# Kernel optimization log

Hardware: AMD Instinct MI355X
Metric: run time of the kernel (lower is better)

The kernel has to match this reference:

```python
import jax, jax.numpy as jnp
import numpy as np

N_NODES = 50000
N_EDGES = 800000
N_FEAT = 128
HIDDEN = 64


def gcn_conv(x, W, b, src, dst, n_nodes):
    """PyG GCNConv: h = D^{-1/2}(A+I)D^{-1/2} (x @ W) + b, with self-loops."""
    h = x @ W  # [N, H] -- linear first, then aggregate (as PyG does)
    # degree including self-loop: deg[i] = 1 + in-degree(i)
    deg = jnp.ones((n_nodes,), dtype=h.dtype).at[dst].add(1.0)
    dinv = jax.lax.rsqrt(deg)  # deg >= 1 so safe
    # edge messages with symmetric normalization
    coef = dinv[src] * dinv[dst]  # [E]
    msg = h[src] * coef[:, None]  # [E, H]  (dominant memory traffic)
    agg = jnp.zeros_like(h).at[dst].add(msg)
    # self-loop contribution: dinv[i]^2 * h[i]
    out = agg + h * (dinv * dinv)[:, None]
    return out + b


def setup_inputs() -> dict:
    key = jax.random.key(0)
    k1, k2, k3, k4 = jax.random.split(key, 4)
    x = jax.random.normal(k1, (N_NODES, N_FEAT), dtype=jnp.float32)
    edge_index = jax.random.randint(k2, (2, N_EDGES), 0, N_NODES, dtype=jnp.int64)
    W1 = jax.random.normal(k3, (N_FEAT, HIDDEN), dtype=jnp.float32) / np.sqrt(N_FEAT)
    b1 = jnp.zeros((HIDDEN,), dtype=jnp.float32)
    W2 = jax.random.normal(k4, (HIDDEN, HIDDEN), dtype=jnp.float32) / np.sqrt(HIDDEN)
    b2 = jnp.zeros((HIDDEN,), dtype=jnp.float32)
    return {"x": x, "edge_index": edge_index, "W1": W1, "b1": b1, "W2": W2, "b2": b2}


def reference(x, edge_index, W1, b1, W2, b2):
    # eval mode: F.dropout(p=0.5, training=False) is identity
    src, dst = edge_index[0], edge_index[1]
    h = gcn_conv(x, W1, b1, src, dst, N_NODES)
    h = jax.nn.relu(h)
    h = gcn_conv(h, W2, b2, src, dst, N_NODES)
    h = jax.nn.relu(h)
    return h
```

## Files before the change

kernel.cpp:

```cpp
#include <hip/hip_runtime.h>
#include <hip/hip_bf16.h>
#include <hip/hip_fp16.h>


#define THREADS 256

__device__ inline int wave_incl_scan(int v, int lane) {
#pragma unroll
    for (int ofs = 1; ofs < 64; ofs <<= 1) {
        int t = __shfl_up(v, ofs, 64);
        if (lane >= ofs) v += t;
    }
    return v;
}

__global__ void k_zero(int4* __restrict__ p, int n4) {
    int i = blockIdx.x * blockDim.x + threadIdx.x;
    if (i < n4) p[i] = make_int4(0, 0, 0, 0);
}

__global__ __launch_bounds__(256)
void k_bin_count(const int* __restrict__ dst, int* __restrict__ bincnt,
                 int n_edges) {
    __shared__ int hist[1024];
    const int tid = threadIdx.x;
    for (int i = tid; i < 1024; i += 256) hist[i] = 0;
    __syncthreads();
    const int base = blockIdx.x * 4096 + tid * 16;
#pragma unroll
    for (int j = 0; j < 4; ++j) {
        int o = base + j * 4;
        if (o + 4 <= n_edges) {
            int4 d = *(const int4*)&dst[o];
            atomicAdd(&hist[d.x >> 6], 1);
            atomicAdd(&hist[d.y >> 6], 1);
            atomicAdd(&hist[d.z >> 6], 1);
            atomicAdd(&hist[d.w >> 6], 1);
        } else {
            for (int t = o; t < n_edges; ++t) atomicAdd(&hist[dst[t] >> 6], 1);
        }
    }
    __syncthreads();
    for (int i = tid; i < 1024; i += 256)
        if (hist[i]) atomicAdd(&bincnt[i], hist[i]);
}

__global__ __launch_bounds__(1024)
void k_bin_scan(const int* __restrict__ bincnt, int* __restrict__ bin_base,
                int* __restrict__ bin_cursor, int nbins) {
    __shared__ int wsum[16];
    const int tid = threadIdx.x;
    const int lane = tid & 63;
    const int wid = tid >> 6;
    int v = (tid < nbins) ? bincnt[tid] : 0;
    int s = wave_incl_scan(v, lane);
    if (lane == 63) wsum[wid] = s;
    __syncthreads();
    if (wid == 0) {
        int t = (lane < 16) ? wsum[lane] : 0;
        int t2 = wave_incl_scan(t, lane);
        if (lane < 16) wsum[lane] = t2;
    }
    __syncthreads();
    int incl = s + ((wid > 0) ? wsum[wid - 1] : 0);
    if (tid < nbins) {
        int excl = incl - v;
        bin_base[tid] = excl;
        bin_cursor[tid] = excl;
    }
    if (tid == 0) bin_base[nbins] = wsum[15];
}

__global__ __launch_bounds__(1024)
void k_bin_scatter(const int* __restrict__ src, const int* __restrict__ dst,
                   int* __restrict__ bin_cursor, unsigned int* __restrict__ edge_binned,
                   int n_edges) {
    __shared__ int cnt[1024];
    __shared__ int lbase[1024];
    __shared__ int gbase[1024];
    __shared__ int run[1024];
    __shared__ int wsum[16];
    __shared__ unsigned int staged[4096];
    __shared__ unsigned short binarr[4096];
    const int tid = threadIdx.x;
    const int lane = tid & 63;
    const int wid = tid >> 6;
    const int base = blockIdx.x * 4096 + tid * 4;
    cnt[tid] = 0;
    run[tid] = 0;
    __syncthreads();

    int dv[4], sv[4];
    int nv = (base < n_edges) ? min(4, n_edges - base) : 0;
    if (nv == 4) {
        int4 a = *(const int4*)&dst[base];
        dv[0] = a.x; dv[1] = a.y; dv[2] = a.z; dv[3] = a.w;
        int4 b = *(const int4*)&src[base];
        sv[0] = b.x; sv[1] = b.y; sv[2] = b.z; sv[3] = b.w;
    } else {
        for (int j = 0; j < nv; ++j) {
            dv[j] = dst[base + j];
            sv[j] = src[base + j];
        }
    }
    for (int j = 0; j < nv; ++j) atomicAdd(&cnt[dv[j] >> 6], 1);
    __syncthreads();
    int mycnt = cnt[tid];
    int s = wave_incl_scan(mycnt, lane);
    if (lane == 63) wsum[wid] = s;
    __syncthreads();
    if (wid == 0) {
        int t = (lane < 16) ? wsum[lane] : 0;
        int t2 = wave_incl_scan(t, lane);
        if (lane < 16) wsum[lane] = t2;
    }
    __syncthreads();
    int incl = s + ((wid > 0) ? wsum[wid - 1] : 0);
    lbase[tid] = incl - mycnt;
    if (mycnt > 0) gbase[tid] = atomicAdd(&bin_cursor[tid], mycnt);
    __syncthreads();
    for (int j = 0; j < nv; ++j) {
        int bn = dv[j] >> 6;
        int rank = atomicAdd(&run[bn], 1);
        int lp = lbase[bn] + rank;
        staged[lp] = ((unsigned)sv[j] << 6) | (unsigned)(dv[j] & 63);
        binarr[lp] = (unsigned short)bn;
    }
    __syncthreads();
    int tot = wsum[15];
    for (int slot = tid; slot < tot; slot += 1024) {
        int bn = binarr[slot];
        edge_binned[gbase[bn] + (slot - lbase[bn])] = staged[slot];
    }
}

__global__ __launch_bounds__(256)
void k_csr_build(const unsigned int* __restrict__ edge_binned,
                 const int* __restrict__ bin_base, int* __restrict__ edge_src,
                 int* __restrict__ offsets, int* __restrict__ degi,
                 float* __restrict__ dinv, int n_nodes) {
    __shared__ int lcnt[64];
    __shared__ int sc[64];
    __shared__ int lcur[64];
    const int b = blockIdx.x;
    const int node0 = b << 6;
    const int tid = threadIdx.x;
    const int ebeg = bin_base[b];
    const int eend = bin_base[b + 1];

    if (tid < 64) lcnt[tid] = 0;
    __syncthreads();
    for (int k = ebeg + tid; k < eend; k += 256)
        atomicAdd(&lcnt[edge_binned[k] & 63u], 1);
    __syncthreads();

    if (tid < 64) sc[tid] = lcnt[tid];
    __syncthreads();
    for (int ofs = 1; ofs < 64; ofs <<= 1) {
        int v = 0;
        if (tid < 64 && tid >= ofs) v = sc[tid - ofs];
        __syncthreads();
        if (tid < 64) sc[tid] += v;
        __syncthreads();
    }
    if (tid < 64) {
        int cntv = lcnt[tid];
        int excl = ebeg + sc[tid] - cntv;
        lcur[tid] = excl;
        int node = node0 + tid;
        if (node < n_nodes) {
            offsets[node] = excl;
            degi[node] = cntv;
            dinv[node] = 1.0f / sqrtf((float)(1 + cntv));
        }
    }
    __syncthreads();
    for (int k = ebeg + tid; k < eend; k += 256) {
        unsigned p = edge_binned[k];
        int pos = atomicAdd(&lcur[p & 63u], 1);
        edge_src[pos] = (int)(p >> 6);
    }
}

template <int K>
__global__ __launch_bounds__(256, 2)
void k_gemm(const float* __restrict__ X, const float* __restrict__ W,
            const float* __restrict__ dinv, __half* __restrict__ H, int n_rows) {
    constexpr int KQ = K / 4;
    constexpr int RSH = (KQ == 32) ? 5 : 4;
    __shared__ float sW[K * 64];
    __shared__ float sX[64 * K];
    const int tid = threadIdx.x;
    const int row0 = blockIdx.x * 64;

#pragma unroll
    for (int it = 0; it < (K * 64 / 4) / THREADS; ++it) {
        int idx = it * THREADS + tid;
        ((float4*)sW)[idx] = ((const float4*)W)[idx];
    }
#pragma unroll
    for (int it = 0; it < (64 * KQ) / THREADS; ++it) {
        int idx = it * THREADS + tid;
        int kq = idx & (KQ - 1);
        int r = idx >> RSH;
        float4 g = make_float4(0.f, 0.f, 0.f, 0.f);
        int grow = row0 + r;
        if (grow < n_rows) g = *(const float4*)&X[(size_t)grow * K + 4 * kq];
        *(float4*)&sX[r * K + ((kq ^ (r & 7)) << 2)] = g;
    }
    __syncthreads();

    const int tx = tid & 15;
    const int ty = tid >> 4;
    float acc[4][4];
#pragma unroll
    for (int i = 0; i < 4; ++i)
#pragma unroll
        for (int j = 0; j < 4; ++j) acc[i][j] = 0.f;

#pragma unroll 2
    for (int k4 = 0; k4 < KQ; ++k4) {
        float4 b0 = *(const float4*)&sW[(4 * k4 + 0) * 64 + 4 * tx];
        float4 b1 = *(const float4*)&sW[(4 * k4 + 1) * 64 + 4 * tx];
        float4 b2 = *(const float4*)&sW[(4 * k4 + 2) * 64 + 4 * tx];
        float4 b3 = *(const float4*)&sW[(4 * k4 + 3) * 64 + 4 * tx];
#pragma unroll
        for (int i = 0; i < 4; ++i) {
            int r = 4 * ty + i;
            float4 a = *(const float4*)&sX[r * K + ((k4 ^ (r & 7)) << 2)];
            acc[i][0] = fmaf(a.x, b0.x, acc[i][0]);
            acc[i][1] = fmaf(a.x, b0.y, acc[i][1]);
            acc[i][2] = fmaf(a.x, b0.z, acc[i][2]);
            acc[i][3] = fmaf(a.x, b0.w, acc[i][3]);
            acc[i][0] = fmaf(a.y, b1.x, acc[i][0]);
            acc[i][1] = fmaf(a.y, b1.y, acc[i][1]);
            acc[i][2] = fmaf(a.y, b1.z, acc[i][2]);
            acc[i][3] = fmaf(a.y, b1.w, acc[i][3]);
            acc[i][0] = fmaf(a.z, b2.x, acc[i][0]);
            acc[i][1] = fmaf(a.z, b2.y, acc[i][1]);
            acc[i][2] = fmaf(a.z, b2.z, acc[i][2]);
            acc[i][3] = fmaf(a.z, b2.w, acc[i][3]);
            acc[i][0] = fmaf(a.w, b3.x, acc[i][0]);
            acc[i][1] = fmaf(a.w, b3.y, acc[i][1]);
            acc[i][2] = fmaf(a.w, b3.z, acc[i][2]);
            acc[i][3] = fmaf(a.w, b3.w, acc[i][3]);
        }
    }

#pragma unroll
    for (int i = 0; i < 4; ++i) {
        int grow = row0 + 4 * ty + i;
        if (grow < n_rows) {
            float dvv = dinv[grow];
            union { __half2 h[2]; uint2 u; } pk;
            pk.h[0] = __floats2half2_rn(acc[i][0] * dvv, acc[i][1] * dvv);
            pk.h[1] = __floats2half2_rn(acc[i][2] * dvv, acc[i][3] * dvv);
            *(uint2*)&H[(size_t)grow * 64 + 4 * tx] = pk.u;
        }
    }
}

__device__ inline void acc_row16(float2 acc[4], uint4 u) {
    const __half2* hp = (const __half2*)&u;
    float2 a = __half22float2(hp[0]);
    float2 b = __half22float2(hp[1]);
    float2 c = __half22float2(hp[2]);
    float2 d = __half22float2(hp[3]);
    acc[0].x += a.x; acc[0].y += a.y;
    acc[1].x += b.x; acc[1].y += b.y;
    acc[2].x += c.x; acc[2].y += c.y;
    acc[3].x += d.x; acc[3].y += d.y;
}

__device__ inline void gather_node(float2 acc[4], const __half* __restrict__ Hp,
                                   int node, int l, const int* __restrict__ offsets,
                                   const int* __restrict__ degi,
                                   const int* __restrict__ edge_src) {
    acc[0] = make_float2(0.f, 0.f); acc[1] = make_float2(0.f, 0.f);
    acc[2] = make_float2(0.f, 0.f); acc[3] = make_float2(0.f, 0.f);
    acc_row16(acc, *(const uint4*)(Hp + ((size_t)node << 6) + (l << 3)));
    int start = offsets[node];
    int cnt = degi[node];
    int k = 0;
    for (; k + 8 <= cnt; k += 8) {
        int s0 = edge_src[start + k];
        int s1 = edge_src[start + k + 1];
        int s2 = edge_src[start + k + 2];
        int s3 = edge_src[start + k + 3];
        int s4 = edge_src[start + k + 4];
        int s5 = edge_src[start + k + 5];
        int s6 = edge_src[start + k + 6];
        int s7 = edge_src[start + k + 7];
        uint4 u0 = *(const uint4*)(Hp + ((size_t)s0 << 6) + (l << 3));
        uint4 u1 = *(const uint4*)(Hp + ((size_t)s1 << 6) + (l << 3));
        uint4 u2 = *(const uint4*)(Hp + ((size_t)s2 << 6) + (l << 3));
        uint4 u3 = *(const uint4*)(Hp + ((size_t)s3 << 6) + (l << 3));
        uint4 u4 = *(const uint4*)(Hp + ((size_t)s4 << 6) + (l << 3));
        uint4 u5 = *(const uint4*)(Hp + ((size_t)s5 << 6) + (l << 3));
        uint4 u6 = *(const uint4*)(Hp + ((size_t)s6 << 6) + (l << 3));
        uint4 u7 = *(const uint4*)(Hp + ((size_t)s7 << 6) + (l << 3));
        acc_row16(acc, u0); acc_row16(acc, u1); acc_row16(acc, u2); acc_row16(acc, u3);
        acc_row16(acc, u4); acc_row16(acc, u5); acc_row16(acc, u6); acc_row16(acc, u7);
    }
    for (; k + 4 <= cnt; k += 4) {
        int s0 = edge_src[start + k];
        int s1 = edge_src[start + k + 1];
        int s2 = edge_src[start + k + 2];
        int s3 = edge_src[start + k + 3];
        uint4 u0 = *(const uint4*)(Hp + ((size_t)s0 << 6) + (l << 3));
        uint4 u1 = *(const uint4*)(Hp + ((size_t)s1 << 6) + (l << 3));
        uint4 u2 = *(const uint4*)(Hp + ((size_t)s2 << 6) + (l << 3));
        uint4 u3 = *(const uint4*)(Hp + ((size_t)s3 << 6) + (l << 3));
        acc_row16(acc, u0); acc_row16(acc, u1); acc_row16(acc, u2); acc_row16(acc, u3);
    }
    for (; k < cnt; ++k) {
        int s0 = edge_src[start + k];
        acc_row16(acc, *(const uint4*)(Hp + ((size_t)s0 << 6) + (l << 3)));
    }
}

__global__ __launch_bounds__(256)
void k_agg_gemm(const __half* __restrict__ Hp, const int* __restrict__ offsets,
                const int* __restrict__ degi, const int* __restrict__ edge_src,
                const float* __restrict__ dinv, const float* __restrict__ b1,
                const float* __restrict__ W2, __half* __restrict__ H2, int n_nodes) {
    __shared__ float sX[32 * 64];
    __shared__ float sW[64 * 64];
    const int tid = threadIdx.x;
    const int node0 = blockIdx.x * 32;

#pragma unroll
    for (int it = 0; it < 4; ++it)
        ((float4*)sW)[it * 256 + tid] = ((const float4*)W2)[it * 256 + tid];

    {
        const int r = tid >> 3;
        const int l = tid & 7;
        const int node = node0 + r;
        float v[8];
        if (node < n_nodes) {
            float2 acc[4];
            gather_node(acc, Hp, node, l, offsets, degi, edge_src);
            float dv = dinv[node];
            const float* bp = b1 + (l << 3);
            v[0] = fmaxf(fmaf(acc[0].x, dv, bp[0]), 0.f);
            v[1] = fmaxf(fmaf(acc[0].y, dv, bp[1]), 0.f);
            v[2] = fmaxf(fmaf(acc[1].x, dv, bp[2]), 0.f);
            v[3] = fmaxf(fmaf(acc[1].y, dv, bp[3]), 0.f);
            v[4] = fmaxf(fmaf(acc[2].x, dv, bp[4]), 0.f);
            v[5] = fmaxf(fmaf(acc[2].y, dv, bp[5]), 0.f);
            v[6] = fmaxf(fmaf(acc[3].x, dv, bp[6]), 0.f);
            v[7] = fmaxf(fmaf(acc[3].y, dv, bp[7]), 0.f);
        } else {
#pragma unroll
            for (int j = 0; j < 8; ++j) v[j] = 0.f;
        }
        *(float4*)&sX[r * 64 + (((2 * l + 0) ^ (r & 7)) << 2)] =
            make_float4(v[0], v[1], v[2], v[3]);
        *(float4*)&sX[r * 64 + (((2 * l + 1) ^ (r & 7)) << 2)] =
            make_float4(v[4], v[5], v[6], v[7]);
    }
    __syncthreads();

    const int tx = tid & 15;
    const int ty = tid >> 4;
    float acc2[2][4];
#pragma unroll
    for (int i = 0; i < 2; ++i)
#pragma unroll
        for (int j = 0; j < 4; ++j) acc2[i][j] = 0.f;

#pragma unroll 2
    for (int k4 = 0; k4 < 16; ++k4) {
        float4 b0 = *(const float4*)&sW[(4 * k4 + 0) * 64 + 4 * tx];
        float4 b1v = *(const float4*)&sW[(4 * k4 + 1) * 64 + 4 * tx];
        float4 b2 = *(const float4*)&sW[(4 * k4 + 2) * 64 + 4 * tx];
        float4 b3 = *(const float4*)&sW[(4 * k4 + 3) * 64 + 4 * tx];
#pragma unroll
        for (int i = 0; i < 2; ++i) {
            int r = 2 * ty + i;
            float4 a = *(const float4*)&sX[r * 64 + ((k4 ^ (r & 7)) << 2)];
            acc2[i][0] = fmaf(a.x, b0.x, acc2[i][0]);
            acc2[i][1] = fmaf(a.x, b0.y, acc2[i][1]);
            acc2[i][2] = fmaf(a.x, b0.z, acc2[i][2]);
            acc2[i][3] = fmaf(a.x, b0.w, acc2[i][3]);
            acc2[i][0] = fmaf(a.y, b1v.x, acc2[i][0]);
            acc2[i][1] = fmaf(a.y, b1v.y, acc2[i][1]);
            acc2[i][2] = fmaf(a.y, b1v.z, acc2[i][2]);
            acc2[i][3] = fmaf(a.y, b1v.w, acc2[i][3]);
            acc2[i][0] = fmaf(a.z, b2.x, acc2[i][0]);
            acc2[i][1] = fmaf(a.z, b2.y, acc2[i][1]);
            acc2[i][2] = fmaf(a.z, b2.z, acc2[i][2]);
            acc2[i][3] = fmaf(a.z, b2.w, acc2[i][3]);
            acc2[i][0] = fmaf(a.w, b3.x, acc2[i][0]);
            acc2[i][1] = fmaf(a.w, b3.y, acc2[i][1]);
            acc2[i][2] = fmaf(a.w, b3.z, acc2[i][2]);
            acc2[i][3] = fmaf(a.w, b3.w, acc2[i][3]);
        }
    }

#pragma unroll
    for (int i = 0; i < 2; ++i) {
        int grow = node0 + 2 * ty + i;
        if (grow < n_nodes) {
            float dvv = dinv[grow];
            union { __half2 h[2]; uint2 u; } pk;
            pk.h[0] = __floats2half2_rn(acc2[i][0] * dvv, acc2[i][1] * dvv);
            pk.h[1] = __floats2half2_rn(acc2[i][2] * dvv, acc2[i][3] * dvv);
            *(uint2*)&H2[(size_t)grow * 64 + 4 * tx] = pk.u;
        }
    }
}

__global__ void k_gather_agg(const __half* __restrict__ Hp, const int* __restrict__ offsets,
                             const int* __restrict__ degi, const int* __restrict__ edge_src,
                             const float* __restrict__ dinv, const float* __restrict__ b,
                             float* __restrict__ out, int n_nodes) {
    int node = blockIdx.x * (THREADS / 8) + (threadIdx.x >> 3);
    if (node >= n_nodes) return;
    int l = threadIdx.x & 7;
    float2 acc[4];
    gather_node(acc, Hp, node, l, offsets, degi, edge_src);

    float dv = dinv[node];
    const float* bp = b + (l << 3);
    float* op = out + ((size_t)node << 6) + (l << 3);
    float4 o0, o1;
    o0.x = fmaxf(fmaf(acc[0].x, dv, bp[0]), 0.0f);
    o0.y = fmaxf(fmaf(acc[0].y, dv, bp[1]), 0.0f);
    o0.z = fmaxf(fmaf(acc[1].x, dv, bp[2]), 0.0f);
    o0.w = fmaxf(fmaf(acc[1].y, dv, bp[3]), 0.0f);
    o1.x = fmaxf(fmaf(acc[2].x, dv, bp[4]), 0.0f);
    o1.y = fmaxf(fmaf(acc[2].y, dv, bp[5]), 0.0f);
    o1.z = fmaxf(fmaf(acc[3].x, dv, bp[6]), 0.0f);
    o1.w = fmaxf(fmaf(acc[3].y, dv, bp[7]), 0.0f);
    *(float4*)op = o0;
    *(float4*)(op + 4) = o1;
}

extern "C" void kernel_launch(void* const* d_in, const int* in_sizes, int n_in,
                              void* d_out, int out_size, void* d_ws, size_t ws_size,
                              hipStream_t stream) {
    const float* x  = (const float*)d_in[0];
    const int*   ei = (const int*)d_in[1];
    const float* W1 = (const float*)d_in[2];
    const float* b1 = (const float*)d_in[3];
    const float* W2 = (const float*)d_in[4];
    const float* b2 = (const float*)d_in[5];
    float* out = (float*)d_out;

    const int n_feat  = 128;
    const int n_nodes = in_sizes[0] / n_feat;
    const int n_edges = in_sizes[1] / 2;
    const int* src = ei;
    const int* dst = ei + n_edges;
    const int nbins = (n_nodes + 63) >> 6;

    const size_t n_pad = (size_t)((n_nodes + 63) & ~63);
    float* dinv        = (float*)d_ws;
    int*   degi        = (int*)(dinv + n_pad);
    int*   offsets     = degi + n_pad;
    int*   bincnt      = offsets + n_pad;
    int*   bin_base    = bincnt + 1024;
    int*   bin_cursor  = bin_base + 1040;
    const size_t e_pad = (size_t)((n_edges + 63) & ~63);
    unsigned int* edge_binned = (unsigned int*)(bin_cursor + 1024);
    int*   edge_src    = (int*)(edge_binned + e_pad);
    __half* h1         = (__half*)(edge_src + e_pad);
    __half* h2         = h1 + (size_t)n_nodes * 64;

    k_zero<<<1, THREADS, 0, stream>>>((int4*)bincnt, 256);
    k_bin_count<<<(n_edges + 4095) / 4096, THREADS, 0, stream>>>(dst, bincnt, n_edges);
    k_bin_scan<<<1, 1024, 0, stream>>>(bincnt, bin_base, bin_cursor, nbins);
    k_bin_scatter<<<(n_edges + 4095) / 4096, 1024, 0, stream>>>(
        src, dst, bin_cursor, edge_binned, n_edges);
    k_csr_build<<<nbins, THREADS, 0, stream>>>(
        edge_binned, bin_base, edge_src, offsets, degi, dinv, n_nodes);

    const int gemm_blocks = (n_nodes + 63) / 64;
    const int fuse_blocks = (n_nodes + 31) / 32;
    const int agg_blocks = (n_nodes + (THREADS / 8) - 1) / (THREADS / 8);

    k_gemm<128><<<gemm_blocks, THREADS, 0, stream>>>(x, W1, dinv, h1, n_nodes);
    k_agg_gemm<<<fuse_blocks, THREADS, 0, stream>>>(
        h1, offsets, degi, edge_src, dinv, b1, W2, h2, n_nodes);
    k_gather_agg<<<agg_blocks, THREADS, 0, stream>>>(
        h2, offsets, degi, edge_src, dinv, b2, out, n_nodes);
}
```

Measured before the change: 103.5 us.

## Widen CSR bins to 128 nodes, drop zero kernel, software-pipeline gather indices

Bin width rises from 64 to 128 nodes, which halves the bin count and gives fewer, larger csr_build blocks. The zero-fill kernel and the global atomics in bin_count are removed: each block writes its own partial histogram, and the scan kernel sums these per bin. The gather loop is rewritten to prefetch the next 8 edge indices while the current 8 feature rows load, overlapping the index-load latency. The trade-off is a serial per-thread reduction over about 196 partials in the scan kernel and a larger workspace for the partial histograms.

```diff
diff --git a/kernel.cpp b/kernel.cpp
--- a/kernel.cpp
+++ b/kernel.cpp
@@ -4,6 +4,9 @@
 
 
 #define THREADS 256
+#define BINSH 7
+#define BINW (1 << BINSH)
+#define MAXBINS 512
 
 __device__ inline int wave_incl_scan(int v, int lane) {
 #pragma unroll
@@ -14,17 +17,12 @@
     return v;
 }
 
-__global__ void k_zero(int4* __restrict__ p, int n4) {
-    int i = blockIdx.x * blockDim.x + threadIdx.x;
-    if (i < n4) p[i] = make_int4(0, 0, 0, 0);
-}
-
 __global__ __launch_bounds__(256)
-void k_bin_count(const int* __restrict__ dst, int* __restrict__ bincnt,
+void k_bin_count(const int* __restrict__ dst, int* __restrict__ partials,
                  int n_edges) {
-    __shared__ int hist[1024];
-    const int tid = threadIdx.x;
-    for (int i = tid; i < 1024; i += 256) hist[i] = 0;
+    __shared__ int hist[MAXBINS];
+    const int tid = threadIdx.x;
+    for (int i = tid; i < MAXBINS; i += 256) hist[i] = 0;
     __syncthreads();
     const int base = blockIdx.x * 4096 + tid * 16;
 #pragma unroll
@@ -32,27 +30,31 @@
         int o = base + j * 4;
         if (o + 4 <= n_edges) {
             int4 d = *(const int4*)&dst[o];
-            atomicAdd(&hist[d.x >> 6], 1);
-            atomicAdd(&hist[d.y >> 6], 1);
-            atomicAdd(&hist[d.z >> 6], 1);
-            atomicAdd(&hist[d.w >> 6], 1);
+            atomicAdd(&hist[d.x >> BINSH], 1);
+            atomicAdd(&hist[d.y >> BINSH], 1);
+            atomicAdd(&hist[d.z >> BINSH], 1);
+            atomicAdd(&hist[d.w >> BINSH], 1);
         } else {
-            for (int t = o; t < n_edges; ++t) atomicAdd(&hist[dst[t] >> 6], 1);
-        }
-    }
-    __syncthreads();
-    for (int i = tid; i < 1024; i += 256)
-        if (hist[i]) atomicAdd(&bincnt[i], hist[i]);
+            for (int t = o; t < n_edges; ++t) atomicAdd(&hist[dst[t] >> BINSH], 1);
+        }
+    }
+    __syncthreads();
+    int* outp = partials + blockIdx.x * MAXBINS;
+    for (int i = tid; i < MAXBINS; i += 256) outp[i] = hist[i];
 }
 
 __global__ __launch_bounds__(1024)
-void k_bin_scan(const int* __restrict__ bincnt, int* __restrict__ bin_base,
-                int* __restrict__ bin_cursor, int nbins) {
+void k_bin_scan(const int* __restrict__ partials, int nblk,
+                int* __restrict__ bin_base, int* __restrict__ bin_cursor,
+                int nbins) {
     __shared__ int wsum[16];
     const int tid = threadIdx.x;
     const int lane = tid & 63;
     const int wid = tid >> 6;
-    int v = (tid < nbins) ? bincnt[tid] : 0;
+    int v = 0;
+    if (tid < MAXBINS) {
+        for (int b = 0; b < nblk; ++b) v += partials[b * MAXBINS + tid];
+    }
     int s = wave_incl_scan(v, lane);
     if (lane == 63) wsum[wid] = s;
     __syncthreads();
@@ -103,7 +105,7 @@
             sv[j] = src[base + j];
         }
     }
-    for (int j = 0; j < nv; ++j) atomicAdd(&cnt[dv[j] >> 6], 1);
+    for (int j = 0; j < nv; ++j) atomicAdd(&cnt[dv[j] >> BINSH], 1);
     __syncthreads();
     int mycnt = cnt[tid];
     int s = wave_incl_scan(mycnt, lane);
@@ -120,10 +122,10 @@
     if (mycnt > 0) gbase[tid] = atomicAdd(&bin_cursor[tid], mycnt);
     __syncthreads();
     for (int j = 0; j < nv; ++j) {
-        int bn = dv[j] >> 6;
+        int bn = dv[j] >> BINSH;
         int rank = atomicAdd(&run[bn], 1);
         int lp = lbase[bn] + rank;
-        staged[lp] = ((unsigned)sv[j] << 6) | (unsigned)(dv[j] & 63);
+        staged[lp] = ((unsigned)sv[j] << BINSH) | (unsigned)(dv[j] & (BINW - 1));
         binarr[lp] = (unsigned short)bn;
     }
     __syncthreads();
@@ -139,31 +141,31 @@
                  const int* __restrict__ bin_base, int* __restrict__ edge_src,
                  int* __restrict__ offsets, int* __restrict__ degi,
                  float* __restrict__ dinv, int n_nodes) {
-    __shared__ int lcnt[64];
-    __shared__ int sc[64];
-    __shared__ int lcur[64];
+    __shared__ int lcnt[BINW];
+    __shared__ int sc[BINW];
+    __shared__ int lcur[BINW];
     const int b = blockIdx.x;
-    const int node0 = b << 6;
+    const int node0 = b << BINSH;
     const int tid = threadIdx.x;
     const int ebeg = bin_base[b];
     const int eend = bin_base[b + 1];
 
-    if (tid < 64) lcnt[tid] = 0;
+    if (tid < BINW) lcnt[tid] = 0;
     __syncthreads();
     for (int k = ebeg + tid; k < eend; k += 256)
-        atomicAdd(&lcnt[edge_binned[k] & 63u], 1);
-    __syncthreads();
-
-    if (tid < 64) sc[tid] = lcnt[tid];
-    __syncthreads();
-    for (int ofs = 1; ofs < 64; ofs <<= 1) {
+        atomicAdd(&lcnt[edge_binned[k] & (BINW - 1u)], 1);
+    __syncthreads();
+
+    if (tid < BINW) sc[tid] = lcnt[tid];
+    __syncthreads();
+    for (int ofs = 1; ofs < BINW; ofs <<= 1) {
         int v = 0;
-        if (tid < 64 && tid >= ofs) v = sc[tid - ofs];
+        if (tid < BINW && tid >= ofs) v = sc[tid - ofs];
         __syncthreads();
-        if (tid < 64) sc[tid] += v;
+        if (tid < BINW) sc[tid] += v;
         __syncthreads();
     }
-    if (tid < 64) {
+    if (tid < BINW) {
         int cntv = lcnt[tid];
         int excl = ebeg + sc[tid] - cntv;
         lcur[tid] = excl;
@@ -177,8 +179,8 @@
     __syncthreads();
     for (int k = ebeg + tid; k < eend; k += 256) {
         unsigned p = edge_binned[k];
-        int pos = atomicAdd(&lcur[p & 63u], 1);
-        edge_src[pos] = (int)(p >> 6);
+        int pos = atomicAdd(&lcur[p & (BINW - 1u)], 1);
+        edge_src[pos] = (int)(p >> BINSH);
     }
 }
 
@@ -279,39 +281,32 @@
     acc[0] = make_float2(0.f, 0.f); acc[1] = make_float2(0.f, 0.f);
     acc[2] = make_float2(0.f, 0.f); acc[3] = make_float2(0.f, 0.f);
     acc_row16(acc, *(const uint4*)(Hp + ((size_t)node << 6) + (l << 3)));
-    int start = offsets[node];
-    int cnt = degi[node];
+    const int start = offsets[node];
+    const int cnt = degi[node];
     int k = 0;
-    for (; k + 8 <= cnt; k += 8) {
-        int s0 = edge_src[start + k];
-        int s1 = edge_src[start + k + 1];
-        int s2 = edge_src[start + k + 2];
-        int s3 = edge_src[start + k + 3];
-        int s4 = edge_src[start + k + 4];
-        int s5 = edge_src[start + k + 5];
-        int s6 = edge_src[start + k + 6];
-        int s7 = edge_src[start + k + 7];
-        uint4 u0 = *(const uint4*)(Hp + ((size_t)s0 << 6) + (l << 3));
-        uint4 u1 = *(const uint4*)(Hp + ((size_t)s1 << 6) + (l << 3));
-        uint4 u2 = *(const uint4*)(Hp + ((size_t)s2 << 6) + (l << 3));
-        uint4 u3 = *(const uint4*)(Hp + ((size_t)s3 << 6) + (l << 3));
-        uint4 u4 = *(const uint4*)(Hp + ((size_t)s4 << 6) + (l << 3));
-        uint4 u5 = *(const uint4*)(Hp + ((size_t)s5 << 6) + (l << 3));
-        uint4 u6 = *(const uint4*)(Hp + ((size_t)s6 << 6) + (l << 3));
-        uint4 u7 = *(const uint4*)(Hp + ((size_t)s7 << 6) + (l << 3));
-        acc_row16(acc, u0); acc_row16(acc, u1); acc_row16(acc, u2); acc_row16(acc, u3);
-        acc_row16(acc, u4); acc_row16(acc, u5); acc_row16(acc, u6); acc_row16(acc, u7);
-    }
-    for (; k + 4 <= cnt; k += 4) {
-        int s0 = edge_src[start + k];
-        int s1 = edge_src[start + k + 1];
-        int s2 = edge_src[start + k + 2];
-        int s3 = edge_src[start + k + 3];
-        uint4 u0 = *(const uint4*)(Hp + ((size_t)s0 << 6) + (l << 3));
-        uint4 u1 = *(const uint4*)(Hp + ((size_t)s1 << 6) + (l << 3));
-        uint4 u2 = *(const uint4*)(Hp + ((size_t)s2 << 6) + (l << 3));
-        uint4 u3 = *(const uint4*)(Hp + ((size_t)s3 << 6) + (l << 3));
-        acc_row16(acc, u0); acc_row16(acc, u1); acc_row16(acc, u2); acc_row16(acc, u3);
+    if (cnt >= 8) {
+        int s[8];
+#pragma unroll
+        for (int j = 0; j < 8; ++j) s[j] = edge_src[start + j];
+        for (; k + 16 <= cnt; k += 8) {
+            uint4 u[8];
+#pragma unroll
+            for (int j = 0; j < 8; ++j)
+                u[j] = *(const uint4*)(Hp + ((size_t)s[j] << 6) + (l << 3));
+#pragma unroll
+            for (int j = 0; j < 8; ++j) s[j] = edge_src[start + k + 8 + j];
+#pragma unroll
+            for (int j = 0; j < 8; ++j) acc_row16(acc, u[j]);
+        }
+        {
+            uint4 u[8];
+#pragma unroll
+            for (int j = 0; j < 8; ++j)
+                u[j] = *(const uint4*)(Hp + ((size_t)s[j] << 6) + (l << 3));
+#pragma unroll
+            for (int j = 0; j < 8; ++j) acc_row16(acc, u[j]);
+            k += 8;
+        }
     }
     for (; k < cnt; ++k) {
         int s0 = edge_src[start + k];
@@ -454,26 +449,25 @@
     const int n_edges = in_sizes[1] / 2;
     const int* src = ei;
     const int* dst = ei + n_edges;
-    const int nbins = (n_nodes + 63) >> 6;
+    const int nbins = (n_nodes + BINW - 1) >> BINSH;
+    const int nblk  = (n_edges + 4095) / 4096;
 
     const size_t n_pad = (size_t)((n_nodes + 63) & ~63);
     float* dinv        = (float*)d_ws;
     int*   degi        = (int*)(dinv + n_pad);
     int*   offsets     = degi + n_pad;
-    int*   bincnt      = offsets + n_pad;
-    int*   bin_base    = bincnt + 1024;
-    int*   bin_cursor  = bin_base + 1040;
+    int*   bin_base    = offsets + n_pad;
+    int*   bin_cursor  = bin_base + 640;
+    int*   partials    = bin_cursor + 512;
     const size_t e_pad = (size_t)((n_edges + 63) & ~63);
-    unsigned int* edge_binned = (unsigned int*)(bin_cursor + 1024);
+    unsigned int* edge_binned = (unsigned int*)(partials + (size_t)nblk * MAXBINS);
     int*   edge_src    = (int*)(edge_binned + e_pad);
     __half* h1         = (__half*)(edge_src + e_pad);
     __half* h2         = h1 + (size_t)n_nodes * 64;
 
-    k_zero<<<1, THREADS, 0, stream>>>((int4*)bincnt, 256);
-    k_bin_count<<<(n_edges + 4095) / 4096, THREADS, 0, stream>>>(dst, bincnt, n_edges);
-    k_bin_scan<<<1, 1024, 0, stream>>>(bincnt, bin_base, bin_cursor, nbins);
-    k_bin_scatter<<<(n_edges + 4095) / 4096, 1024, 0, stream>>>(
-        src, dst, bin_cursor, edge_binned, n_edges);
+    k_bin_count<<<nblk, THREADS, 0, stream>>>(dst, partials, n_edges);
+    k_bin_scan<<<1, 1024, 0, stream>>>(partials, nblk, bin_base, bin_cursor, nbins);
+    k_bin_scatter<<<nblk, 1024, 0, stream>>>(src, dst, bin_cursor, edge_binned, n_edges);
     k_csr_build<<<nbins, THREADS, 0, stream>>>(
         edge_binned, bin_base, edge_src, offsets, degi, dinv, n_nodes);
 
```

After: 123.4 us. 1.19x slower.
